# Optimization experiments

Hardware: AMD Instinct MI355X
Metric: run time of the kernel (lower is better)

Reference implementation:

```python
import jax, jax.numpy as jnp
import numpy as np

B, C, N, K = 4, 192, 8192, 16
C_OUT = 192


def _gather_nodes(xs, idx):
    # xs: [B, C, N], idx: [B, N, K] -> [B, C, N, K]
    return jax.vmap(lambda xb, ib: xb[:, ib])(xs, idx)


def setup_inputs() -> dict:
    key = jax.random.key(0)
    k1, k2, k3 = jax.random.split(key, 3)
    x = jax.random.normal(k1, (B, C, N, 1), dtype=jnp.float32)
    x_0 = jnp.zeros((B, C, N, 1), dtype=jnp.float32)  # unused by forward, kept for interface
    edge_index = jax.random.randint(k2, (2, B, N, K), 0, N, dtype=jnp.int32)
    # 1x1 Conv2d(2C -> C_OUT) weight flattened to [C_OUT, 2C]
    W = jax.random.normal(k3, (C_OUT, 2 * C), dtype=jnp.float32) / np.sqrt(2 * C)
    b = jnp.zeros((C_OUT,), dtype=jnp.float32)
    return {"x": x, "x_0": x_0, "edge_index": edge_index, "W": W, "b": b}


def reference(x, x_0, edge_index, W, b):
    xs = x[..., 0]                       # [B, C, N]
    x_i = _gather_nodes(xs, edge_index[1])   # centers  [B, C, N, K]
    x_j = _gather_nodes(xs, edge_index[0])   # neighbors [B, C, N, K]
    rel = jnp.max(x_j - x_i, axis=-1)        # max-relative [B, C, N]
    y = jnp.concatenate([xs, rel], axis=1)   # [B, 2C, N]
    out = jnp.einsum('oc,bcn->bon', W, y) + b[None, :, None]  # 1x1 conv
    out = jax.nn.relu(out)
    return out[..., None]                # [B, C_OUT, N, 1]
```

## Files before the change

### kernel.cpp

```cpp
#include <hip/hip_runtime.h>
#include <hip/hip_fp16.h>

#define B_    4
#define C_    192
#define N_    8192
#define K_    16
#define O_    192
#define TWOC_ 384
#define BN_   (B_ * N_)

typedef __attribute__((ext_vector_type(8))) _Float16 half8;
typedef __attribute__((ext_vector_type(4))) _Float16 half4v;
typedef __attribute__((ext_vector_type(2))) _Float16 half2v;
typedef __attribute__((ext_vector_type(4))) float floatx4;
typedef __attribute__((ext_vector_type(4))) float fvec4;
typedef __attribute__((ext_vector_type(4))) int   ivec4;
typedef __attribute__((ext_vector_type(4))) unsigned int uvec4;
typedef __attribute__((ext_vector_type(2))) unsigned int uvec2;

__global__ __launch_bounds__(256) void k_prep(const float* __restrict__ x,
                                              const float* __restrict__ W,
                                              unsigned short* __restrict__ xt,
                                              unsigned short* __restrict__ xc,
                                              unsigned short* __restrict__ Wb) {
    int bid = blockIdx.x;
    int tid = threadIdx.x;

    if (bid >= 6144) {
        int base = ((bid - 6144) * 256 + tid) * 16;
        union { unsigned short u[16]; uvec4 v[2]; } o;
#pragma unroll
        for (int q = 0; q < 16; q += 4) {
            fvec4 f = __builtin_nontemporal_load((const fvec4*)(W + base + q));
            union { _Float16 h; unsigned short s; } c;
            c.h = (_Float16)f.x; o.u[q + 0] = c.s;
            c.h = (_Float16)f.y; o.u[q + 1] = c.s;
            c.h = (_Float16)f.z; o.u[q + 2] = c.s;
            c.h = (_Float16)f.w; o.u[q + 3] = c.s;
        }
        *(uvec4*)(Wb + base)     = o.v[0];
        *(uvec4*)(Wb + base + 8) = o.v[1];
        return;
    }

    __shared__ float tile[32][33];
    int xcd  = bid & 7;
    int b    = xcd >> 1;
    int half = xcd & 1;
    int slot = bid >> 3;
    int ct   = slot >> 7;
    int nt   = half * 128 + (slot & 127);
    int c0 = ct * 32, n0 = nt * 32;

    int cc  = tid >> 3;
    int nn4 = (tid & 7) * 4;
    const float* xp = x + ((size_t)b * C_ + c0 + cc) * N_ + n0 + nn4;
    fvec4 v = __builtin_nontemporal_load((const fvec4*)xp);

    {
        union { _Float16 h[4]; uvec2 u; } pc;
        pc.h[0] = (_Float16)v.x;
        pc.h[1] = (_Float16)v.y;
        pc.h[2] = (_Float16)v.z;
        pc.h[3] = (_Float16)v.w;
        *(uvec2*)(xc + ((size_t)b * C_ + c0 + cc) * N_ + n0 + nn4) = pc.u;
    }

    tile[nn4 + 0][cc] = v.x;
    tile[nn4 + 1][cc] = v.y;
    tile[nn4 + 2][cc] = v.z;
    tile[nn4 + 3][cc] = v.w;
    __syncthreads();

#pragma unroll
    for (int i = 0; i < 2; i++) {
        int id  = i * 256 + tid;
        int row = id >> 4;
        int ch2 = id & 15;
        union { _Float16 h[2]; unsigned int u; } p;
        p.h[0] = (_Float16)tile[row][ch2 * 2];
        p.h[1] = (_Float16)tile[row][ch2 * 2 + 1];
        *(unsigned int*)(xt + ((size_t)b * N_ + n0 + row) * C_ + c0 + ch2 * 2) = p.u;
    }
}

__global__ __launch_bounds__(256) void k_gather(const unsigned short* __restrict__ xc,
                                                const int* __restrict__ eidx,
                                                unsigned short* __restrict__ rt) {
    __shared__ unsigned int lds[2 * N_];

    int bid  = blockIdx.x;
    int xcd  = bid & 7;
    int b    = xcd >> 1;
    int hq   = xcd & 1;
    int rest = bid >> 3;
    int s    = rest >> 1;
    int qq   = rest & 1;
    int nq   = hq * 2 + qq;
    int c0   = s * 4;
    int nbase = nq * 2048;
    int tid  = threadIdx.x;

#pragma unroll
    for (int p = 0; p < 2; p++) {
        const unsigned short* ra = xc + ((size_t)b * C_ + c0 + 2 * p) * N_;
        const unsigned short* rb = ra + N_;
#pragma unroll
        for (int i = 0; i < 4; i++) {
            int n0 = i * 2048 + tid * 8;
            uvec4 A = *(const uvec4*)(ra + n0);
            uvec4 Bv = *(const uvec4*)(rb + n0);
#pragma unroll
            for (int q = 0; q < 4; q++) {
                unsigned a = A[q], bb = Bv[q];
                unsigned lo = (a & 0xffffu) | (bb << 16);
                unsigned hi = (a >> 16) | (bb & 0xffff0000u);
                uvec2 w2 = {lo, hi};
                *(uvec2*)&lds[p * N_ + n0 + q * 2] = w2;
            }
        }
    }
    __syncthreads();

    const int* e0 = eidx + (size_t)b * N_ * K_;
    const int* e1 = e0 + (size_t)BN_ * K_;
    unsigned short* rto = rt + (size_t)b * N_ * C_ + c0;

#pragma unroll 2
    for (int i = 0; i < 8; i++) {
        int n = nbase + i * 256 + tid;
        ivec4 J[4], I[4];
#pragma unroll
        for (int kq = 0; kq < 4; kq++) {
            J[kq] = *(const ivec4*)(e0 + (size_t)n * K_ + kq * 4);
            I[kq] = *(const ivec4*)(e1 + (size_t)n * K_ + kq * 4);
        }
        half2v m0 = {(_Float16)-65504.f, (_Float16)-65504.f};
        half2v m1 = m0;
#pragma unroll
        for (int kq = 0; kq < 4; kq++)
#pragma unroll
            for (int e = 0; e < 4; e++) {
                int jn  = J[kq][e];
                int in_ = I[kq][e];
                union { unsigned u; half2v h; } j0, j1, i0, i1;
                j0.u = lds[jn];        j1.u = lds[N_ + jn];
                i0.u = lds[in_];       i1.u = lds[N_ + in_];
                m0 = __builtin_elementwise_max(m0, j0.h - i0.h);
                m1 = __builtin_elementwise_max(m1, j1.h - i1.h);
            }
        union { half2v h; unsigned u; } o0, o1;
        o0.h = m0; o1.h = m1;
        uvec2 ov = {o0.u, o1.u};
        *(uvec2*)(rto + (size_t)n * C_) = ov;
    }
}

__global__ __launch_bounds__(256) void k_conv(const unsigned short* __restrict__ xt,
                                              const unsigned short* __restrict__ rt,
                                              const unsigned short* __restrict__ Wb,
                                              const float* __restrict__ bias,
                                              float* __restrict__ out) {
    __shared__ __align__(16) unsigned short ytile[64 * TWOC_];
    char* yb = (char*)ytile;

    int bid  = blockIdx.x;
    int xcd  = bid & 7;
    int b    = xcd >> 1;
    int slot = bid >> 3;
    int n0   = ((xcd & 1) * 64 + slot) * 64;

    int tid  = threadIdx.x;
    int wave = tid >> 6;
    int lane = tid & 63;
    int m16  = lane & 15;
    int quad = lane >> 4;

    const unsigned short* xsrc = xt + ((size_t)b * N_ + n0) * C_;
    const unsigned short* rsrc = rt + ((size_t)b * N_ + n0) * C_;
#pragma unroll
    for (int i = 0; i < 6; i++) {
        int id = i * 256 + tid;
        int row = id / 24, chunk = id % 24;
        int sw = (row & 7) << 4;
        half8 vx = *(const half8*)(xsrc + (size_t)row * C_ + chunk * 8);
        half8 vr = *(const half8*)(rsrc + (size_t)row * C_ + chunk * 8);
        *(half8*)(yb + row * 768 + ((chunk * 16) ^ sw))       = vx;
        *(half8*)(yb + row * 768 + 384 + ((chunk * 16) ^ sw)) = vr;
    }
    __syncthreads();

    const unsigned short* wbase = Wb + (size_t)(wave * 48 + m16) * TWOC_ + quad * 8;

    floatx4 acc[3][4];
#pragma unroll
    for (int i = 0; i < 3; i++)
#pragma unroll
        for (int j = 0; j < 4; j++) acc[i][j] = (floatx4){0.f, 0.f, 0.f, 0.f};

#pragma unroll 2
    for (int kt = 0; kt < 12; kt++) {
        half8 wf[3], yf[4];
#pragma unroll
        for (int i = 0; i < 3; i++)
            wf[i] = *(const half8*)(wbase + (size_t)(i * 16) * TWOC_ + kt * 32);
#pragma unroll
        for (int j = 0; j < 4; j++) {
            int row = j * 16 + m16;
            yf[j] = *(const half8*)(yb + row * 768 + ((kt * 64 + quad * 16) ^ ((row & 7) << 4)));
        }
#pragma unroll
        for (int i = 0; i < 3; i++)
#pragma unroll
            for (int j = 0; j < 4; j++)
                acc[i][j] = __builtin_amdgcn_mfma_f32_16x16x32_f16(wf[i], yf[j], acc[i][j], 0, 0, 0);
    }

#pragma unroll
    for (int i = 0; i < 3; i++) {
#pragma unroll
        for (int r = 0; r < 4; r++) {
            int o = wave * 48 + i * 16 + quad * 4 + r;
            float bv = bias[o];
#pragma unroll
            for (int j = 0; j < 4; j++) {
                int n = n0 + j * 16 + m16;
                __builtin_nontemporal_store(fmaxf(acc[i][j][r] + bv, 0.f),
                                            &out[((size_t)b * O_ + o) * N_ + n]);
            }
        }
    }
}

extern "C" void kernel_launch(void* const* d_in, const int* in_sizes, int n_in,
                              void* d_out, int out_size, void* d_ws, size_t ws_size,
                              hipStream_t stream) {
    const float* x    = (const float*)d_in[0];
    const int*   eidx = (const int*)d_in[2];
    const float* W    = (const float*)d_in[3];
    const float* bias = (const float*)d_in[4];
    float*       out  = (float*)d_out;

    unsigned short* Wb = (unsigned short*)d_ws;
    unsigned short* xt = (unsigned short*)((char*)d_ws + 147456);
    unsigned short* xc = (unsigned short*)((char*)d_ws + 12730368);
    unsigned short* rt = (unsigned short*)((char*)d_ws + 25313280);

    k_prep<<<dim3(6162), dim3(256), 0, stream>>>(x, W, xt, xc, Wb);
    k_gather<<<dim3(768), dim3(256), 0, stream>>>(xc, eidx, rt);
    k_conv<<<dim3(512), dim3(256), 0, stream>>>(xt, rt, Wb, bias, out);
}
```

Before: 144.3 us.

## Interleave 4-channel slices for gather and halve edge-index reloads

The prep kernel now writes x in a layout where each group of 4 channels is packed per node in 8 bytes. The gather kernel copies a slice straight into LDS and reads each neighbor with a single 64-bit LDS access. Each block covers twice as many nodes, so the edge indices are reloaded half as often across channel slices. Each thread now processes 16 consecutive nodes, which makes the edge-index loads strided across lanes and may reduce coalescing.

```diff
diff --git a/kernel.cpp b/kernel.cpp
--- a/kernel.cpp
+++ b/kernel.cpp
@@ -8,10 +8,10 @@
 #define O_    192
 #define TWOC_ 384
 #define BN_   (B_ * N_)
+#define NSL_  48
 
 typedef __attribute__((ext_vector_type(8))) _Float16 half8;
 typedef __attribute__((ext_vector_type(4))) _Float16 half4v;
-typedef __attribute__((ext_vector_type(2))) _Float16 half2v;
 typedef __attribute__((ext_vector_type(4))) float floatx4;
 typedef __attribute__((ext_vector_type(4))) float fvec4;
 typedef __attribute__((ext_vector_type(4))) int   ivec4;
@@ -21,7 +21,7 @@
 __global__ __launch_bounds__(256) void k_prep(const float* __restrict__ x,
                                               const float* __restrict__ W,
                                               unsigned short* __restrict__ xt,
-                                              unsigned short* __restrict__ xc,
+                                              unsigned short* __restrict__ xg,
                                               unsigned short* __restrict__ Wb) {
     int bid = blockIdx.x;
     int tid = threadIdx.x;
@@ -56,16 +56,6 @@
     int nn4 = (tid & 7) * 4;
     const float* xp = x + ((size_t)b * C_ + c0 + cc) * N_ + n0 + nn4;
     fvec4 v = __builtin_nontemporal_load((const fvec4*)xp);
-
-    {
-        union { _Float16 h[4]; uvec2 u; } pc;
-        pc.h[0] = (_Float16)v.x;
-        pc.h[1] = (_Float16)v.y;
-        pc.h[2] = (_Float16)v.z;
-        pc.h[3] = (_Float16)v.w;
-        *(uvec2*)(xc + ((size_t)b * C_ + c0 + cc) * N_ + n0 + nn4) = pc.u;
-    }
-
     tile[nn4 + 0][cc] = v.x;
     tile[nn4 + 1][cc] = v.y;
     tile[nn4 + 2][cc] = v.z;
@@ -82,77 +72,68 @@
         p.h[1] = (_Float16)tile[row][ch2 * 2 + 1];
         *(unsigned int*)(xt + ((size_t)b * N_ + n0 + row) * C_ + c0 + ch2 * 2) = p.u;
     }
-}
-
-__global__ __launch_bounds__(256) void k_gather(const unsigned short* __restrict__ xc,
+
+    {
+        int sl  = tid >> 5;
+        int row = tid & 31;
+        union { _Float16 h[4]; uvec2 u; } p;
+#pragma unroll
+        for (int c = 0; c < 4; c++) p.h[c] = (_Float16)tile[row][sl * 4 + c];
+        *(uvec2*)(xg + ((size_t)(b * NSL_ + ct * 8 + sl) * N_ + n0 + row) * 4) = p.u;
+    }
+}
+
+__global__ __launch_bounds__(256) void k_gather(const unsigned short* __restrict__ xg,
                                                 const int* __restrict__ eidx,
                                                 unsigned short* __restrict__ rt) {
-    __shared__ unsigned int lds[2 * N_];
-
-    int bid  = blockIdx.x;
-    int xcd  = bid & 7;
-    int b    = xcd >> 1;
-    int hq   = xcd & 1;
-    int rest = bid >> 3;
-    int s    = rest >> 1;
-    int qq   = rest & 1;
-    int nq   = hq * 2 + qq;
-    int c0   = s * 4;
-    int nbase = nq * 2048;
-    int tid  = threadIdx.x;
-
-#pragma unroll
-    for (int p = 0; p < 2; p++) {
-        const unsigned short* ra = xc + ((size_t)b * C_ + c0 + 2 * p) * N_;
-        const unsigned short* rb = ra + N_;
-#pragma unroll
-        for (int i = 0; i < 4; i++) {
-            int n0 = i * 2048 + tid * 8;
-            uvec4 A = *(const uvec4*)(ra + n0);
-            uvec4 Bv = *(const uvec4*)(rb + n0);
-#pragma unroll
-            for (int q = 0; q < 4; q++) {
-                unsigned a = A[q], bb = Bv[q];
-                unsigned lo = (a & 0xffffu) | (bb << 16);
-                unsigned hi = (a >> 16) | (bb & 0xffff0000u);
-                uvec2 w2 = {lo, hi};
-                *(uvec2*)&lds[p * N_ + n0 + q * 2] = w2;
-            }
-        }
+    __shared__ uvec2 lds2[N_];
+
+    int bid = blockIdx.x;
+    int xcd = bid & 7;
+    int b   = xcd >> 1;
+    int nh  = xcd & 1;
+    int s   = bid >> 3;
+    int tid = threadIdx.x;
+
+    const unsigned short* src = xg + (size_t)(b * NSL_ + s) * N_ * 4;
+#pragma unroll
+    for (int i = 0; i < 16; i++) {
+        int idx = i * 256 + tid;
+        uvec4 v = *(const uvec4*)(src + (size_t)idx * 8);
+        *(uvec4*)&lds2[idx * 2] = v;
     }
     __syncthreads();
 
+    int nbase = nh * 4096;
     const int* e0 = eidx + (size_t)b * N_ * K_;
     const int* e1 = e0 + (size_t)BN_ * K_;
-    unsigned short* rto = rt + (size_t)b * N_ * C_ + c0;
+    unsigned short* rto = rt + (size_t)b * N_ * C_ + s * 4;
 
 #pragma unroll 2
-    for (int i = 0; i < 8; i++) {
-        int n = nbase + i * 256 + tid;
+    for (int nn = 0; nn < 16; nn++) {
+        int n = nbase + tid * 16 + nn;
+        const int* ej = e0 + (size_t)n * K_;
+        const int* ei = e1 + (size_t)n * K_;
         ivec4 J[4], I[4];
 #pragma unroll
-        for (int kq = 0; kq < 4; kq++) {
-            J[kq] = *(const ivec4*)(e0 + (size_t)n * K_ + kq * 4);
-            I[kq] = *(const ivec4*)(e1 + (size_t)n * K_ + kq * 4);
-        }
-        half2v m0 = {(_Float16)-65504.f, (_Float16)-65504.f};
-        half2v m1 = m0;
-#pragma unroll
-        for (int kq = 0; kq < 4; kq++)
+        for (int q = 0; q < 4; q++) {
+            J[q] = *(const ivec4*)(ej + q * 4);
+            I[q] = *(const ivec4*)(ei + q * 4);
+        }
+        half4v m;
+#pragma unroll
+        for (int q = 0; q < 4; q++)
 #pragma unroll
             for (int e = 0; e < 4; e++) {
-                int jn  = J[kq][e];
-                int in_ = I[kq][e];
-                union { unsigned u; half2v h; } j0, j1, i0, i1;
-                j0.u = lds[jn];        j1.u = lds[N_ + jn];
-                i0.u = lds[in_];       i1.u = lds[N_ + in_];
-                m0 = __builtin_elementwise_max(m0, j0.h - i0.h);
-                m1 = __builtin_elementwise_max(m1, j1.h - i1.h);
+                union { uvec2 u; half4v h; } jv, iv;
+                jv.u = lds2[J[q][e]];
+                iv.u = lds2[I[q][e]];
+                half4v d = jv.h - iv.h;
+                m = (q == 0 && e == 0) ? d : __builtin_elementwise_max(m, d);
             }
-        union { half2v h; unsigned u; } o0, o1;
-        o0.h = m0; o1.h = m1;
-        uvec2 ov = {o0.u, o1.u};
-        *(uvec2*)(rto + (size_t)n * C_) = ov;
+        union { half4v h; uvec2 u; } o;
+        o.h = m;
+        *(uvec2*)(rto + (size_t)n * C_) = o.u;
     }
 }
 
@@ -243,10 +224,10 @@
 
     unsigned short* Wb = (unsigned short*)d_ws;
     unsigned short* xt = (unsigned short*)((char*)d_ws + 147456);
-    unsigned short* xc = (unsigned short*)((char*)d_ws + 12730368);
+    unsigned short* xg = (unsigned short*)((char*)d_ws + 12730368);
     unsigned short* rt = (unsigned short*)((char*)d_ws + 25313280);
 
-    k_prep<<<dim3(6162), dim3(256), 0, stream>>>(x, W, xt, xc, Wb);
-    k_gather<<<dim3(768), dim3(256), 0, stream>>>(xc, eidx, rt);
+    k_prep<<<dim3(6162), dim3(256), 0, stream>>>(x, W, xt, xg, Wb);
+    k_gather<<<dim3(384), dim3(256), 0, stream>>>(xg, eidx, rt);
     k_conv<<<dim3(512), dim3(256), 0, stream>>>(xt, rt, Wb, bias, out);
 }
```

Result: slower. 157.0 us (+8.8%).
